# Optimization experiments

Hardware: AMD Instinct MI355X
Metric: run time of the kernel (lower is better)

The kernel has to match this reference:

```python
import jax, jax.numpy as jnp
import numpy as np

R = 128          # voxel grid resolution
B = 2            # batch size
NPB = 250_000    # active voxels per batch item
N = B * NPB      # total active voxels
C_IN = 32        # in_nchannel
C0 = 32          # enc_ch[0] = out_nchannel
C1 = 32          # enc_ch[1]
EPS = 1e-5


def _build_neighbor_maps():
    """Build Minkowski-style kernel maps: for each kernel offset k and output
    voxel n, nmap[k, n] = index of the input voxel at coord+offset, or -1."""
    rng = np.random.default_rng(0)
    keys_list = []
    for b in range(B):
        flat = rng.choice(R ** 3, NPB, replace=False).astype(np.int64)
        keys_list.append(b * (R ** 3) + np.sort(flat))
    keys = np.concatenate(keys_list)  # globally sorted (batch-major)
    local = keys % (R ** 3)
    bidx = keys // (R ** 3)
    x = local // (R * R)
    y = (local // R) % R
    z = local % R

    def make(offsets):
        nmap = np.full((len(offsets), N), -1, dtype=np.int32)
        for k, (dx, dy, dz) in enumerate(offsets):
            nx, ny, nz = x + dx, y + dy, z + dz
            valid = (nx >= 0) & (nx < R) & (ny >= 0) & (ny < R) & (nz >= 0) & (nz < R)
            nkey = bidx * (R ** 3) + nx * R * R + ny * R + nz
            pos = np.searchsorted(keys, nkey)
            pos_c = np.clip(pos, 0, N - 1)
            valid &= keys[pos_c] == nkey
            nmap[k] = np.where(valid, pos_c, -1)
        return nmap

    off3 = [(dx, dy, dz) for dx in (-1, 0, 1) for dy in (-1, 0, 1) for dz in (-1, 0, 1)]
    off2 = [(dx, dy, dz) for dx in (0, 1) for dy in (0, 1) for dz in (0, 1)]
    return jnp.asarray(make(off3)), jnp.asarray(make(off2))


def setup_inputs() -> dict:
    key = jax.random.key(0)
    ks = jax.random.split(key, 8)
    nmap3, nmap2 = _build_neighbor_maps()
    s3_in = 1.0 / np.sqrt(27 * C_IN)
    s2 = 1.0 / np.sqrt(8 * C0)
    s3 = 1.0 / np.sqrt(27 * C1)
    return {
        "feats": jax.random.normal(ks[0], (N, C_IN), jnp.float32),
        "W1": jax.random.normal(ks[1], (27, C_IN, C0), jnp.float32) * s3_in,
        "g1": jnp.ones((C0,), jnp.float32),
        "b1": jnp.zeros((C0,), jnp.float32),
        "W2": jax.random.normal(ks[2], (8, C0, C1), jnp.float32) * s2,
        "g2": jnp.ones((C1,), jnp.float32),
        "b2": jnp.zeros((C1,), jnp.float32),
        "W3": jax.random.normal(ks[3], (27, C1, C1), jnp.float32) * s3,
        "g3": jnp.ones((C1,), jnp.float32),
        "b3": jnp.zeros((C1,), jnp.float32),
        "nmap3": nmap3,
        "nmap2": nmap2,
    }


def sparse_conv(feats, nmap, W):
    """MinkowskiConvolution (no bias): gather neighbors per kernel offset,
    GEMM with that offset's weight, accumulate. Loop is over the fixed,
    small kernel volume (8 or 27), not over data."""
    out = jnp.zeros((feats.shape[0], W.shape[-1]), feats.dtype)
    for k in range(W.shape[0]):
        idx = nmap[k]
        g = jnp.where((idx >= 0)[:, None], feats[jnp.maximum(idx, 0)], 0.0)
        out = out + g @ W[k]
    return out


def bn_elu(x, gamma, beta):
    # MinkowskiBatchNorm over all active voxels (training-mode stats) + ELU
    mean = jnp.mean(x, axis=0)
    var = jnp.var(x, axis=0)
    xn = (x - mean) * jax.lax.rsqrt(var + EPS)
    return jax.nn.elu(xn * gamma + beta)


def reference(feats, W1, g1, b1, W2, g2, b2, W3, g3, b3, nmap3, nmap2):
    # enc_block_s1: conv k=3 s=1 -> BN -> ELU
    h = bn_elu(sparse_conv(feats, nmap3, W1), g1, b1)
    # enc_block_s1s2: conv k=2 s=1 -> BN -> ELU -> conv k=3 -> BN -> ELU
    h = bn_elu(sparse_conv(h, nmap2, W2), g2, b2)
    h = bn_elu(sparse_conv(h, nmap3, W3), g3, b3)
    return h
```

## Files before the change

kernel.cpp:

```cpp
#include <hip/hip_runtime.h>


typedef short shortx8 __attribute__((ext_vector_type(8)));
typedef float floatx4 __attribute__((ext_vector_type(4)));

__device__ __forceinline__ float bf2f(unsigned short h) {
    unsigned u = ((unsigned)h) << 16;
    return __builtin_bit_cast(float, u);
}
__device__ __forceinline__ unsigned short f2bf(float f) {
    unsigned u = __builtin_bit_cast(unsigned, f);
    return (unsigned short)((u + 0x7fffu + ((u >> 16) & 1u)) >> 16);
}

__global__ void detect_dtype(const unsigned* __restrict__ g1, int* __restrict__ flag) {
    if (threadIdx.x == 0) *flag = (g1[0] == 0x3F800000u) ? 1 : 0;
}

__global__ __launch_bounds__(256) void prep_w_all(
    const void* __restrict__ W1_, const void* __restrict__ W2_,
    const void* __restrict__ W3_, unsigned short* __restrict__ Wg,
    const int* __restrict__ flag)
{
    int o = blockIdx.x * 256 + threadIdx.x;
    if (o >= 62 * 1024) return;
    const void* W; int lo;
    if (o < 27648)      { W = W1_; lo = o; }
    else if (o < 35840) { W = W2_; lo = o - 27648; }
    else                { W = W3_; lo = o - 35840; }
    int j = lo & 7, lane = (lo >> 3) & 63, f = (lo >> 9) & 1, k = lo >> 10;
    int col = lane & 15, quad = lane >> 4;
    int src = k * 1024 + (quad * 8 + j) * 32 + f * 16 + col;
    unsigned short v = *flag ? f2bf(((const float*)W)[src])
                             : ((const unsigned short*)W)[src];
    Wg[o] = v;
}

__global__ __launch_bounds__(256) void normalize_feats(
    const void* __restrict__ in_, unsigned short* __restrict__ out,
    int total, const int* __restrict__ flag)
{
    int i = (blockIdx.x * 256 + threadIdx.x) * 8;
    if (i >= total) return;
    if (*flag) {
        const float* in = (const float*)in_;
        floatx4 a = *(const floatx4*)(in + i);
        floatx4 b = *(const floatx4*)(in + i + 4);
        unsigned o[4];
        o[0] = (unsigned)f2bf(a[0]) | ((unsigned)f2bf(a[1]) << 16);
        o[1] = (unsigned)f2bf(a[2]) | ((unsigned)f2bf(a[3]) << 16);
        o[2] = (unsigned)f2bf(b[0]) | ((unsigned)f2bf(b[1]) << 16);
        o[3] = (unsigned)f2bf(b[2]) | ((unsigned)f2bf(b[3]) << 16);
        uint4 ov = {o[0], o[1], o[2], o[3]};
        *(uint4*)(out + i) = ov;
    } else {
        *(uint4*)(out + i) = *(const uint4*)((const unsigned short*)in_ + i);
    }
}

template <int KV>
__global__ __launch_bounds__(512, 4) void conv_stats(
    const unsigned short* __restrict__ feats,
    const unsigned short* __restrict__ Wg,
    const int* __restrict__ nmap,
    unsigned short* __restrict__ xout,
    float* __restrict__ stat,
    int N)
{
    __shared__ unsigned short Wl[KV * 1024];
    __shared__ float red[512];

    const int tid = threadIdx.x;
    for (int i = tid; i < KV * 128; i += 512)
        ((uint4*)Wl)[i] = ((const uint4*)Wg)[i];
    __syncthreads();

    const int lane = tid & 63, wave = tid >> 6;
    const int col = lane & 15, quad = lane >> 4;
    const int m0 = (blockIdx.x * 8 + wave) * 64;

    floatx4 accA[4], accB[4];
#pragma unroll
    for (int t = 0; t < 4; ++t) {
        accA[t] = {0.f, 0.f, 0.f, 0.f};
        accB[t] = {0.f, 0.f, 0.f, 0.f};
    }

    if (m0 < N) {
        int rown[4];
#pragma unroll
        for (int t = 0; t < 4; ++t) rown[t] = m0 + t * 16 + col;

        int idxb[2][4];
        shortx8 ab[2][4];

#pragma unroll
        for (int t = 0; t < 4; ++t)
            idxb[0][t] = (rown[t] < N) ? nmap[rown[t]] : -1;
#pragma unroll
        for (int t = 0; t < 4; ++t) {
            shortx8 a = {0, 0, 0, 0, 0, 0, 0, 0};
            int id = idxb[0][t];
            if (id >= 0) a = *(const shortx8*)(feats + (size_t)id * 32 + quad * 8);
            ab[0][t] = a;
        }
        if (KV > 1) {
#pragma unroll
            for (int t = 0; t < 4; ++t)
                idxb[1][t] = (rown[t] < N) ? nmap[N + rown[t]] : -1;
        }

#pragma unroll
        for (int k = 0; k < KV; ++k) {
            const int cur = k & 1, nxt = (k + 1) & 1;
            if (k + 1 < KV) {
#pragma unroll
                for (int t = 0; t < 4; ++t) {
                    shortx8 a = {0, 0, 0, 0, 0, 0, 0, 0};
                    int id = idxb[nxt][t];
                    if (id >= 0) a = *(const shortx8*)(feats + (size_t)id * 32 + quad * 8);
                    ab[nxt][t] = a;
                }
            }
            if (k + 2 < KV) {
#pragma unroll
                for (int t = 0; t < 4; ++t)
                    idxb[cur][t] = (rown[t] < N) ? nmap[(k + 2) * N + rown[t]] : -1;
            }
            shortx8 b0 = *(const shortx8*)(Wl + k * 1024 + lane * 8);
            shortx8 b1 = *(const shortx8*)(Wl + k * 1024 + 512 + lane * 8);
#pragma unroll
            for (int t = 0; t < 4; ++t) {
                accA[t] = __builtin_amdgcn_mfma_f32_16x16x32_bf16(ab[cur][t], b0, accA[t], 0, 0, 0);
                accB[t] = __builtin_amdgcn_mfma_f32_16x16x32_bf16(ab[cur][t], b1, accB[t], 0, 0, 0);
            }
        }

#pragma unroll
        for (int t = 0; t < 4; ++t) {
            int rbase = m0 + t * 16 + quad * 4;
#pragma unroll
            for (int r = 0; r < 4; ++r) {
                int row = rbase + r;
                if (row < N) {
                    xout[row * 32 + col]      = f2bf(accA[t][r]);
                    xout[row * 32 + col + 16] = f2bf(accB[t][r]);
                }
            }
        }
    }

    float s0 = 0.f, s1 = 0.f, q0 = 0.f, q1 = 0.f;
#pragma unroll
    for (int t = 0; t < 4; ++t) {
#pragma unroll
        for (int r = 0; r < 4; ++r) {
            s0 += accA[t][r]; q0 += accA[t][r] * accA[t][r];
            s1 += accB[t][r]; q1 += accB[t][r] * accB[t][r];
        }
    }
    s0 += __shfl_xor(s0, 16); s0 += __shfl_xor(s0, 32);
    s1 += __shfl_xor(s1, 16); s1 += __shfl_xor(s1, 32);
    q0 += __shfl_xor(q0, 16); q0 += __shfl_xor(q0, 32);
    q1 += __shfl_xor(q1, 16); q1 += __shfl_xor(q1, 32);

    if (lane < 16) {
        float* rw = red + wave * 64;
        rw[col]      = s0;
        rw[col + 16] = s1;
        rw[col + 32] = q0;
        rw[col + 48] = q1;
    }
    __syncthreads();
    if (tid < 64) {
        float v = 0.f;
#pragma unroll
        for (int w = 0; w < 8; ++w) v += red[tid + w * 64];
        atomicAdd(stat + tid, v);
    }
}

__global__ __launch_bounds__(256) void bn_elu_apply(
    const unsigned short* __restrict__ x,
    const float* __restrict__ stat,
    const void* __restrict__ g_,
    const void* __restrict__ b_,
    void* __restrict__ out_,
    int total, int N, int finalout,
    const int* __restrict__ flag)
{
    __shared__ float ps[64];
    int tid = threadIdx.x;
    if (tid < 32) {
        int f = *flag;
        float gv = f ? ((const float*)g_)[tid] : bf2f(((const unsigned short*)g_)[tid]);
        float bv = f ? ((const float*)b_)[tid] : bf2f(((const unsigned short*)b_)[tid]);
        float invN = 1.0f / (float)N;
        float mean = stat[tid] * invN;
        float var  = fmaxf(stat[32 + tid] * invN - mean * mean, 0.0f);
        float sc   = gv * rsqrtf(var + 1e-5f);
        ps[tid]      = sc;
        ps[32 + tid] = bv - mean * sc;
    }
    __syncthreads();

    int i = (blockIdx.x * 256 + tid) * 8;
    if (i >= total) return;

    uint4 v = *(const uint4*)(x + i);
    int c0 = i & 31;
    unsigned w[4] = {v.x, v.y, v.z, v.w};
    float y[8];
#pragma unroll
    for (int j = 0; j < 4; ++j) {
        int c = c0 + 2 * j;
        float f0 = bf2f((unsigned short)(w[j] & 0xffffu));
        float f1 = bf2f((unsigned short)(w[j] >> 16));
        float y0 = f0 * ps[c]     + ps[32 + c];
        float y1 = f1 * ps[c + 1] + ps[32 + c + 1];
        y[2*j]     = y0 > 0.f ? y0 : (__expf(y0) - 1.f);
        y[2*j + 1] = y1 > 0.f ? y1 : (__expf(y1) - 1.f);
    }

    if (finalout && *flag) {
        float* o = (float*)out_ + i;
        floatx4 o0 = {y[0], y[1], y[2], y[3]};
        floatx4 o1 = {y[4], y[5], y[6], y[7]};
        *(floatx4*)o = o0;
        *(floatx4*)(o + 4) = o1;
    } else {
        unsigned o[4];
#pragma unroll
        for (int j = 0; j < 4; ++j)
            o[j] = (unsigned)f2bf(y[2*j]) | ((unsigned)f2bf(y[2*j + 1]) << 16);
        uint4 ov = {o[0], o[1], o[2], o[3]};
        *(uint4*)((unsigned short*)out_ + i) = ov;
    }
}

extern "C" void kernel_launch(void* const* d_in, const int* in_sizes, int n_in,
                              void* d_out, int out_size, void* d_ws, size_t ws_size,
                              hipStream_t stream)
{
    const void* feats = d_in[0];
    const void* W1    = d_in[1];
    const void* g1    = d_in[2];
    const void* b1    = d_in[3];
    const void* W2    = d_in[4];
    const void* g2    = d_in[5];
    const void* b2    = d_in[6];
    const void* W3    = d_in[7];
    const void* g3    = d_in[8];
    const void* b3    = d_in[9];
    const int* nmap3  = (const int*)d_in[10];
    const int* nmap2  = (const int*)d_in[11];

    const int N = in_sizes[0] / 32;
    const int total = N * 32;

    char* ws = (char*)d_ws;
    float* stat0 = (float*)(ws);
    float* stat1 = (float*)(ws + 256);
    float* stat2 = (float*)(ws + 512);
    int*   flagD = (int*)(ws + 768);
    unsigned short* Wg  = (unsigned short*)(ws + 4096);
    unsigned short* Wg1 = Wg;
    unsigned short* Wg2 = Wg + 27648;
    unsigned short* Wg3 = Wg + 35840;
    unsigned short* xbuf = (unsigned short*)(ws + 131072);
    unsigned short* hbuf = (unsigned short*)d_out;

    hipMemsetAsync(d_ws, 0, 1024, stream);
    detect_dtype<<<1, 64, 0, stream>>>((const unsigned*)g1, flagD);

    prep_w_all<<<(62 * 1024 + 255) / 256, 256, 0, stream>>>(W1, W2, W3, Wg, flagD);
    normalize_feats<<<(total / 8 + 255) / 256, 256, 0, stream>>>(feats, hbuf, total, flagD);

    const int cblocks = (N + 511) / 512;
    const int ablocks = (total / 8 + 255) / 256;

    conv_stats<27><<<cblocks, 512, 0, stream>>>(hbuf, Wg1, nmap3, xbuf, stat0, N);
    bn_elu_apply<<<ablocks, 256, 0, stream>>>(xbuf, stat0, g1, b1, hbuf, total, N, 0, flagD);

    conv_stats<8><<<cblocks, 512, 0, stream>>>(hbuf, Wg2, nmap2, xbuf, stat1, N);
    bn_elu_apply<<<ablocks, 256, 0, stream>>>(xbuf, stat1, g2, b2, hbuf, total, N, 0, flagD);

    conv_stats<27><<<cblocks, 512, 0, stream>>>(hbuf, Wg3, nmap3, xbuf, stat2, N);
    bn_elu_apply<<<ablocks, 256, 0, stream>>>(xbuf, stat2, g3, b3, d_out, total, N, 1, flagD);
}
```

Measured before the change: 392.2 us.

## Stage neighbor maps and weights into LDS via async double-buffered chunks

New measurement: 358.9 us. 1.09x faster.

```diff
diff --git a/kernel.cpp b/kernel.cpp
--- a/kernel.cpp
+++ b/kernel.cpp
@@ -11,6 +11,12 @@
 __device__ __forceinline__ unsigned short f2bf(float f) {
     unsigned u = __builtin_bit_cast(unsigned, f);
     return (unsigned short)((u + 0x7fffu + ((u >> 16) & 1u)) >> 16);
+}
+
+__device__ __forceinline__ void gl_lds16(const void* g, void* l) {
+    __builtin_amdgcn_global_load_lds(
+        (const __attribute__((address_space(1))) unsigned*)g,
+        (__attribute__((address_space(3))) unsigned*)l, 16, 0, 0);
 }
 
 __global__ void detect_dtype(const unsigned* __restrict__ g1, int* __restrict__ flag) {
@@ -40,44 +46,63 @@
     const void* __restrict__ in_, unsigned short* __restrict__ out,
     int total, const int* __restrict__ flag)
 {
+    if (!*flag) return;
     int i = (blockIdx.x * 256 + threadIdx.x) * 8;
     if (i >= total) return;
-    if (*flag) {
-        const float* in = (const float*)in_;
-        floatx4 a = *(const floatx4*)(in + i);
-        floatx4 b = *(const floatx4*)(in + i + 4);
-        unsigned o[4];
-        o[0] = (unsigned)f2bf(a[0]) | ((unsigned)f2bf(a[1]) << 16);
-        o[1] = (unsigned)f2bf(a[2]) | ((unsigned)f2bf(a[3]) << 16);
-        o[2] = (unsigned)f2bf(b[0]) | ((unsigned)f2bf(b[1]) << 16);
-        o[3] = (unsigned)f2bf(b[2]) | ((unsigned)f2bf(b[3]) << 16);
-        uint4 ov = {o[0], o[1], o[2], o[3]};
-        *(uint4*)(out + i) = ov;
-    } else {
-        *(uint4*)(out + i) = *(const uint4*)((const unsigned short*)in_ + i);
-    }
+    const float* in = (const float*)in_;
+    floatx4 a = *(const floatx4*)(in + i);
+    floatx4 b = *(const floatx4*)(in + i + 4);
+    unsigned o[4];
+    o[0] = (unsigned)f2bf(a[0]) | ((unsigned)f2bf(a[1]) << 16);
+    o[1] = (unsigned)f2bf(a[2]) | ((unsigned)f2bf(a[3]) << 16);
+    o[2] = (unsigned)f2bf(b[0]) | ((unsigned)f2bf(b[1]) << 16);
+    o[3] = (unsigned)f2bf(b[2]) | ((unsigned)f2bf(b[3]) << 16);
+    uint4 ov = {o[0], o[1], o[2], o[3]};
+    *(uint4*)(out + i) = ov;
 }
 
 template <int KV>
 __global__ __launch_bounds__(512, 4) void conv_stats(
     const unsigned short* __restrict__ feats,
+    const unsigned short* __restrict__ feats_alt,
     const unsigned short* __restrict__ Wg,
     const int* __restrict__ nmap,
     unsigned short* __restrict__ xout,
     float* __restrict__ stat,
-    int N)
-{
-    __shared__ unsigned short Wl[KV * 1024];
-    __shared__ float red[512];
-
-    const int tid = threadIdx.x;
-    for (int i = tid; i < KV * 128; i += 512)
-        ((uint4*)Wl)[i] = ((const uint4*)Wg)[i];
-    __syncthreads();
-
+    int N,
+    const int* __restrict__ flagA)
+{
+    constexpr int CH  = (KV >= 9) ? 9 : KV;
+    constexpr int NCH = KV / CH;
+    static_assert(KV % CH == 0, "chunking assumes CH | KV");
+    constexpr int BUFB = CH * 4096;
+
+    __shared__ __align__(16) char smem[2 * BUFB + 2048];
+    float* red = (float*)(smem + 2 * BUFB);
+
+    const int tid  = threadIdx.x;
     const int lane = tid & 63, wave = tid >> 6;
-    const int col = lane & 15, quad = lane >> 4;
-    const int m0 = (blockIdx.x * 8 + wave) * 64;
+    const int col  = lane & 15, quad = lane >> 4;
+    const int row0 = blockIdx.x * 512;
+    const int m0   = row0 + wave * 64;
+    const unsigned short* A = (*flagA) ? feats_alt : feats;
+
+    auto stage = [&](int c) {
+        const int kc = c * CH;
+        char* buf = smem + (c & 1) * BUFB;
+        for (int s = wave; s < CH * 4; s += 8) {
+            int ki = s >> 2, part = s & 3;
+            if (part < 2) {
+                int r4 = row0 + part * 256 + lane * 4;
+                if (r4 > N - 4) r4 = N - 4;
+                gl_lds16(nmap + (size_t)(kc + ki) * N + r4,
+                         buf + ki * 2048 + part * 1024);
+            } else {
+                gl_lds16(Wg + (kc + ki) * 1024 + (part - 2) * 512 + lane * 8,
+                         buf + CH * 2048 + ki * 2048 + (part - 2) * 1024);
+            }
+        }
+    };
 
     floatx4 accA[4], accB[4];
 #pragma unroll
@@ -86,66 +111,70 @@
         accB[t] = {0.f, 0.f, 0.f, 0.f};
     }
 
-    if (m0 < N) {
-        int rown[4];
-#pragma unroll
-        for (int t = 0; t < 4; ++t) rown[t] = m0 + t * 16 + col;
-
-        int idxb[2][4];
-        shortx8 ab[2][4];
-
-#pragma unroll
-        for (int t = 0; t < 4; ++t)
-            idxb[0][t] = (rown[t] < N) ? nmap[rown[t]] : -1;
-#pragma unroll
-        for (int t = 0; t < 4; ++t) {
-            shortx8 a = {0, 0, 0, 0, 0, 0, 0, 0};
-            int id = idxb[0][t];
-            if (id >= 0) a = *(const shortx8*)(feats + (size_t)id * 32 + quad * 8);
-            ab[0][t] = a;
-        }
-        if (KV > 1) {
-#pragma unroll
-            for (int t = 0; t < 4; ++t)
-                idxb[1][t] = (rown[t] < N) ? nmap[N + rown[t]] : -1;
-        }
-
-#pragma unroll
-        for (int k = 0; k < KV; ++k) {
-            const int cur = k & 1, nxt = (k + 1) & 1;
-            if (k + 1 < KV) {
+    int rown[4];
+#pragma unroll
+    for (int t = 0; t < 4; ++t) rown[t] = m0 + t * 16 + col;
+
+    stage(0);
+    __syncthreads();
+
+    for (int c = 0; c < NCH; ++c) {
+        if (c + 1 < NCH) stage(c + 1);
+        const int* nsl = (const int*)(smem + (c & 1) * BUFB);
+        const unsigned short* wsl =
+            (const unsigned short*)(smem + (c & 1) * BUFB + CH * 2048);
+
+        shortx8 ring[2][4];
+#pragma unroll
+        for (int p = 0; p < 2; ++p) {
+#pragma unroll
+            for (int t = 0; t < 4; ++t) {
+                int id = (rown[t] < N) ? nsl[p * 512 + wave * 64 + t * 16 + col] : -1;
+                shortx8 a = {0, 0, 0, 0, 0, 0, 0, 0};
+                if (id >= 0) a = *(const shortx8*)(A + (size_t)id * 32 + quad * 8);
+                ring[p][t] = a;
+            }
+        }
+
+#pragma unroll
+        for (int kk = 0; kk < CH; ++kk) {
+            shortx8 at[4];
+#pragma unroll
+            for (int t = 0; t < 4; ++t) at[t] = ring[kk & 1][t];
+
+            if (kk + 2 < CH) {
 #pragma unroll
                 for (int t = 0; t < 4; ++t) {
+                    int id = (rown[t] < N)
+                                 ? nsl[(kk + 2) * 512 + wave * 64 + t * 16 + col]
+                                 : -1;
                     shortx8 a = {0, 0, 0, 0, 0, 0, 0, 0};
-                    int id = idxb[nxt][t];
-                    if (id >= 0) a = *(const shortx8*)(feats + (size_t)id * 32 + quad * 8);
-                    ab[nxt][t] = a;
+                    if (id >= 0) a = *(const shortx8*)(A + (size_t)id * 32 + quad * 8);
+                    ring[kk & 1][t] = a;
                 }
             }
-            if (k + 2 < KV) {
-#pragma unroll
-                for (int t = 0; t < 4; ++t)
-                    idxb[cur][t] = (rown[t] < N) ? nmap[(k + 2) * N + rown[t]] : -1;
-            }
-            shortx8 b0 = *(const shortx8*)(Wl + k * 1024 + lane * 8);
-            shortx8 b1 = *(const shortx8*)(Wl + k * 1024 + 512 + lane * 8);
+
+            shortx8 b0 = *(const shortx8*)(wsl + kk * 1024 + lane * 8);
+            shortx8 b1 = *(const shortx8*)(wsl + kk * 1024 + 512 + lane * 8);
 #pragma unroll
             for (int t = 0; t < 4; ++t) {
-                accA[t] = __builtin_amdgcn_mfma_f32_16x16x32_bf16(ab[cur][t], b0, accA[t], 0, 0, 0);
-                accB[t] = __builtin_amdgcn_mfma_f32_16x16x32_bf16(ab[cur][t], b1, accB[t], 0, 0, 0);
-            }
-        }
-
-#pragma unroll
-        for (int t = 0; t < 4; ++t) {
-            int rbase = m0 + t * 16 + quad * 4;
-#pragma unroll
-            for (int r = 0; r < 4; ++r) {
-                int row = rbase + r;
-                if (row < N) {
-                    xout[row * 32 + col]      = f2bf(accA[t][r]);
-                    xout[row * 32 + col + 16] = f2bf(accB[t][r]);
-                }
+                accA[t] = __builtin_amdgcn_mfma_f32_16x16x32_bf16(at[t], b0, accA[t], 0, 0, 0);
+                accB[t] = __builtin_amdgcn_mfma_f32_16x16x32_bf16(at[t], b1, accB[t], 0, 0, 0);
+            }
+            __builtin_amdgcn_sched_barrier(0);
+        }
+        __syncthreads();
+    }
+
+#pragma unroll
+    for (int t = 0; t < 4; ++t) {
+        int rbase = m0 + t * 16 + quad * 4;
+#pragma unroll
+        for (int r = 0; r < 4; ++r) {
+            int row = rbase + r;
+            if (row < N) {
+                xout[row * 32 + col]      = f2bf(accA[t][r]);
+                xout[row * 32 + col + 16] = f2bf(accB[t][r]);
             }
         }
     }
@@ -279,12 +308,15 @@
     const int cblocks = (N + 511) / 512;
     const int ablocks = (total / 8 + 255) / 256;
 
-    conv_stats<27><<<cblocks, 512, 0, stream>>>(hbuf, Wg1, nmap3, xbuf, stat0, N);
+    conv_stats<27><<<cblocks, 512, 0, stream>>>(
+        (const unsigned short*)feats, hbuf, Wg1, nmap3, xbuf, stat0, N, flagD);
     bn_elu_apply<<<ablocks, 256, 0, stream>>>(xbuf, stat0, g1, b1, hbuf, total, N, 0, flagD);
 
-    conv_stats<8><<<cblocks, 512, 0, stream>>>(hbuf, Wg2, nmap2, xbuf, stat1, N);
+    conv_stats<8><<<cblocks, 512, 0, stream>>>(
+        hbuf, hbuf, Wg2, nmap2, xbuf, stat1, N, flagD);
     bn_elu_apply<<<ablocks, 256, 0, stream>>>(xbuf, stat1, g2, b2, hbuf, total, N, 0, flagD);
 
-    conv_stats<27><<<cblocks, 512, 0, stream>>>(hbuf, Wg3, nmap3, xbuf, stat2, N);
+    conv_stats<27><<<cblocks, 512, 0, stream>>>(
+        hbuf, hbuf, Wg3, nmap3, xbuf, stat2, N, flagD);
     bn_elu_apply<<<ablocks, 256, 0, stream>>>(xbuf, stat2, g3, b3, d_out, total, N, 1, flagD);
 }
```
